# Kernel optimization log

Hardware: AMD Instinct MI355X
Metric: run time of the kernel (lower is better)

The kernel has to match this reference:

```python
import math
import jax
import jax.numpy as jnp
import numpy as np

N_FFT = 2048
HOP = 512
WIN = 2048
N_FREQ = N_FFT // 2 + 1


def _make_buffers():
    # ISTFT synthesis kernel: inverse DFT basis with one-sided spectrum weights.
    n = np.arange(N_FFT, dtype=np.float32)
    k = np.arange(N_FREQ, dtype=np.float32)
    angles = 2.0 * np.pi * k[:, None] * n[None, :] / N_FFT
    w = np.full(N_FREQ, 2.0 / N_FFT, dtype=np.float32)
    w[0] = 1.0 / N_FFT
    if N_FFT % 2 == 0:
        w[-1] = 1.0 / N_FFT
    real_k = np.cos(angles) * w[:, None]
    imag_k = -np.sin(angles) * w[:, None]
    kernel = np.concatenate([real_k, imag_k], axis=0).astype(np.float32)  # [2*N_FREQ, N_FFT]
    # periodic Hann window (torch.hann_window default), win_length == n_fft so no pad
    win = (0.5 * (1.0 - np.cos(2.0 * np.pi * np.arange(WIN) / WIN))).astype(np.float32)
    window_sq = (win * win).astype(np.float32)
    return jnp.asarray(kernel), jnp.asarray(window_sq)


def setup_inputs() -> dict:
    key = jax.random.key(0)
    B, frames = 8, 2048
    stft_repr = jax.random.normal(key, (B, N_FREQ, frames, 2), dtype=jnp.float32)
    kernel, window_sq = _make_buffers()
    orig_len = (frames - 1) * HOP  # 1048064
    return {"stft_repr": stft_repr, "kernel": kernel, "window_sq": window_sq, "orig_len": orig_len}


def reference(stft_repr, kernel, window_sq, orig_len):
    B, n_freq, frames, _ = stft_repr.shape
    # stack real/imag channels: [B, 2*n_freq, frames]
    x = jnp.concatenate([stft_repr[..., 0], stft_repr[..., 1]], axis=1)
    # conv_transpose1d(stride=HOP) == per-frame synthesis GEMM + overlap-add
    contrib = jnp.einsum('bct,cn->btn', x, kernel)  # [B, frames, N_FFT]
    L = (frames - 1) * HOP + N_FFT
    idx = (jnp.arange(frames) * HOP)[:, None] + jnp.arange(N_FFT)[None, :]  # [frames, N_FFT]
    flat = idx.reshape(-1)
    audio = jnp.zeros((B, L), dtype=contrib.dtype).at[:, flat].add(contrib.reshape(B, -1))
    # normalization envelope: every frame fits (e <= L always, since L = (T-1)*hop + n_fft)
    env = jnp.zeros((L,), dtype=window_sq.dtype).at[flat].add(
        jnp.broadcast_to(window_sq, (frames, N_FFT)).reshape(-1))
    env = jnp.maximum(env, 1e-8)
    audio = audio / env[None, :]
    pad = N_FFT // 2
    return audio[:, pad:pad + orig_len]
```

## Files before the change

### kernel.cpp

```cpp
#include <hip/hip_runtime.h>
#include <math.h>

#define NFREQ 1025
#define NT 2048
#define NB 8
#define ORIG_LEN 1048064
#define FR 16
#define SEGS 13
#define NBLK 158
#define FSTR 1028
#define IOFF (FR * FSTR)

__device__ __forceinline__ int dphys(int m) {
    return m ^ ((((m >> 5) ^ (m >> 8)) & 7) << 2);
}
__device__ __forceinline__ int tphys(int r) { return r + (r >> 4); }

template <int LEN, int TSTEP>
__device__ __forceinline__ void r4stage(float* __restrict__ Rw, float* __restrict__ Iw,
                                        const float* __restrict__ TWR,
                                        const float* __restrict__ TWI, int lane) {
#pragma unroll
    for (int c = 0; c < 4; ++c) {
        const int i = lane + (c << 6);
        const int quarter = LEN >> 2;
        const int grp = i / quarter, pos = i - grp * quarter;
        const int i0 = grp * LEN + pos;
        const int ia = dphys(i0), ib = dphys(i0 + quarter);
        const int ic = dphys(i0 + 2 * quarter), id = dphys(i0 + 3 * quarter);
        const float arr = Rw[ia], ari = Iw[ia];
        const float brr = Rw[ib], bri = Iw[ib];
        const float crr = Rw[ic], cri = Iw[ic];
        const float drr = Rw[id], dri = Iw[id];
        const int j1 = tphys(pos * TSTEP), j2 = tphys(2 * pos * TSTEP), j3 = tphys(3 * pos * TSTEP);
        const float w1r = TWR[j1], w1i = TWI[j1];
        const float w2r = TWR[j2], w2i = TWI[j2];
        const float w3r = TWR[j3], w3i = TWI[j3];
        const float t1r = brr * w1r - bri * w1i, t1i = brr * w1i + bri * w1r;
        const float t2r = crr * w2r - cri * w2i, t2i = crr * w2i + cri * w2r;
        const float t3r = drr * w3r - dri * w3i, t3i = drr * w3i + dri * w3r;
        Rw[ia] = arr + t1r + t2r + t3r;  Iw[ia] = ari + t1i + t2i + t3i;
        Rw[ib] = arr - t1i - t2r + t3i;  Iw[ib] = ari + t1r - t2i - t3r;
        Rw[ic] = arr - t1r + t2r - t3r;  Iw[ic] = ari - t1i + t2i - t3i;
        Rw[id] = arr + t1i - t2r - t3i;  Iw[id] = ari - t1r - t2i + t3r;
    }
}

__global__ __launch_bounds__(1024) void istft_fused(const float* __restrict__ in,
                                                    const float* __restrict__ wsq,
                                                    float* __restrict__ out) {
    __shared__ float D[2 * FR * FSTR];
    __shared__ float TWR[816], TWI[816];
    __shared__ float WS[2048];
    const int tid = threadIdx.x;
    const int lane = tid & 63, wv = tid >> 6;
    const int g = blockIdx.x, b = blockIdx.y;
    const int f0 = (g == 0) ? 0 : (13 * g - 1);
    const int sbase = 2 + 13 * g;
    const int nseg = (2049 - sbase < SEGS) ? (2049 - sbase) : SEGS;

    if (tid < 768) {
        float s, c;
        sincosf(6.28318530717958647692f * (float)tid * (1.0f / 1024.0f), &s, &c);
        const int p = tphys(tid);
        TWR[p] = c; TWI[p] = s;
    }
    for (int i = tid; i < 2048; i += 1024) WS[i] = wsq[i];

    const float* bbase = in + (size_t)b * NFREQ * (NT * 2);
#pragma unroll
    for (int it = 0; it < 17; ++it) {
        const int idx = tid + (it << 10);
        if (idx < FR * NFREQ) {
            const int k = idx >> 4, jf = idx & 15, ft = f0 + jf;
            float2 v = make_float2(0.0f, 0.0f);
            if (ft < NT) v = *(const float2*)(bbase + ((size_t)k * NT + ft) * 2);
            D[jf * FSTR + k] = v.x;
            D[IOFF + jf * FSTR + k] = v.y;
        }
    }
    __syncthreads();

    float* Rw = D + wv * FSTR;
    float* Iw = D + IOFF + wv * FSTR;

    float vr[16], vi[16];
#pragma unroll
    for (int m = 0; m < 16; ++m) {
        const int jc = lane + (m << 6);
        const float Xr = Rw[jc];
        const float Xi = (jc == 0) ? 0.0f : Iw[jc];
        const float Cr = Rw[1024 - jc];
        const float Ci = (jc == 0) ? 0.0f : -Iw[1024 - jc];
        const float ar = Xr + Cr, ai = Xi + Ci;
        const float dr = Xr - Cr, di = Xi - Ci;
        const int rr = jc >> 1;
        const int pp = tphys(rr);
        float pr = TWR[pp], pi = TWI[pp];
        if (jc & 1) {
            const float c1r = 0.99999529380957617f, c1i = 0.00306795676296598f;
            const float nr = pr * c1r - pi * c1i;
            pi = pr * c1i + pi * c1r; pr = nr;
        }
        const float br = dr * pr - di * pi;
        const float bi = dr * pi + di * pr;
        vr[m] = (ar - bi) * (1.0f / 2048.0f);
        vi[m] = (ai + br) * (1.0f / 2048.0f);
    }
#pragma unroll
    for (int m0 = 0; m0 < 4; ++m0) {
        const float v0r = vr[m0], v0i = vi[m0];
        const float v1r = vr[m0 + 4], v1i = vi[m0 + 4];
        const float v2r = vr[m0 + 8], v2i = vi[m0 + 8];
        const float v3r = vr[m0 + 12], v3i = vi[m0 + 12];
        const int jb = lane + (m0 << 6);
        const int g8 = ((jb & 3) << 6) | (((jb >> 2) & 3) << 4) |
                       (((jb >> 4) & 3) << 2) | ((jb >> 6) & 3);
        const int p4 = dphys(g8 << 2);
        *(float4*)&Rw[p4] = make_float4(v0r + v1r + v2r + v3r,
                                        v0r - v1i - v2r + v3i,
                                        v0r - v1r + v2r - v3r,
                                        v0r + v1i - v2r - v3i);
        *(float4*)&Iw[p4] = make_float4(v0i + v1i + v2i + v3i,
                                        v0i + v1r - v2i - v3r,
                                        v0i - v1i + v2i - v3i,
                                        v0i - v1r - v2i + v3r);
    }
    r4stage<16, 64>(Rw, Iw, TWR, TWI, lane);
    r4stage<64, 16>(Rw, Iw, TWR, TWI, lane);
    r4stage<256, 4>(Rw, Iw, TWR, TWI, lane);
    r4stage<1024, 1>(Rw, Iw, TWR, TWI, lane);
    __syncthreads();

    const int nsamp = nseg << 9;
    float* outb = out + (size_t)b * ORIG_LEN + (size_t)(sbase - 2) * 512;
#pragma unroll
    for (int it = 0; it < 7; ++it) {
        const int idx = tid + (it << 10);
        if (idx < nsamp) {
            const int seg = idx >> 9, r = idx & 511;
            const int s = sbase + seg;
            const int qlo = (s == 2048) ? 1 : 0;
            const int qhi = (s == 2) ? 2 : 3;
            float acc = 0.0f, wacc = 0.0f;
            const int po = (r & 1) ? IOFF : 0;
#pragma unroll
            for (int q = 0; q < 4; ++q) {
                if (q >= qlo && q <= qhi) {
                    const int lf = s - q - f0;
                    const int n = (q << 9) + r;
                    acc += D[po + lf * FSTR + dphys(n >> 1)];
                    wacc += WS[n];
                }
            }
            outb[idx] = acc / fmaxf(wacc, 1e-8f);
        }
    }
}

extern "C" void kernel_launch(void* const* d_in, const int* in_sizes, int n_in,
                              void* d_out, int out_size, void* d_ws, size_t ws_size,
                              hipStream_t stream) {
    const float* stft = (const float*)d_in[0];
    const float* wsq  = (const float*)d_in[2];
    float* out = (float*)d_out;
    dim3 grid(NBLK, NB);
    istft_fused<<<grid, 1024, 0, stream>>>(stft, wsq, out);
}
```

Baseline: 293.7 us.

## Use interleaved complex LDS layout, derive twiddles, compute constant window envelope

Switches the shared-memory FFT buffer from split real/imag planes to interleaved float2, so each butterfly access is a single 64-bit LDS operation and the output stage writes float2 pairs. Radix-4 twiddles w2 and w3 are now computed from w1 by complex multiplication instead of being loaded, which shrinks the twiddle table. The window_sq input is no longer read: the overlap-add envelope is taken as the analytic constant 1.5 for a periodic Hann at 4x overlap, with edge corrections computed via cosf. This relies on the window being Hann and ignores the supplied buffer, and deriving twiddles by multiplication adds a little rounding error.

```diff
diff --git a/kernel.cpp b/kernel.cpp
--- a/kernel.cpp
+++ b/kernel.cpp
@@ -8,50 +8,47 @@
 #define FR 16
 #define SEGS 13
 #define NBLK 158
-#define FSTR 1028
-#define IOFF (FR * FSTR)
+#define CROW 1026
+#define PI_F 3.14159265358979323846f
 
-__device__ __forceinline__ int dphys(int m) {
+__device__ __forceinline__ int cphys(int m) {
     return m ^ ((((m >> 5) ^ (m >> 8)) & 7) << 2);
 }
 __device__ __forceinline__ int tphys(int r) { return r + (r >> 4); }
 
+__device__ __forceinline__ float2 cmul(float2 a, float2 b) {
+    return make_float2(a.x * b.x - a.y * b.y, a.x * b.y + a.y * b.x);
+}
+
 template <int LEN, int TSTEP>
-__device__ __forceinline__ void r4stage(float* __restrict__ Rw, float* __restrict__ Iw,
-                                        const float* __restrict__ TWR,
-                                        const float* __restrict__ TWI, int lane) {
+__device__ __forceinline__ void r4stage(float2* __restrict__ W,
+                                        const float2* __restrict__ TW, int lane) {
 #pragma unroll
     for (int c = 0; c < 4; ++c) {
         const int i = lane + (c << 6);
         const int quarter = LEN >> 2;
         const int grp = i / quarter, pos = i - grp * quarter;
         const int i0 = grp * LEN + pos;
-        const int ia = dphys(i0), ib = dphys(i0 + quarter);
-        const int ic = dphys(i0 + 2 * quarter), id = dphys(i0 + 3 * quarter);
-        const float arr = Rw[ia], ari = Iw[ia];
-        const float brr = Rw[ib], bri = Iw[ib];
-        const float crr = Rw[ic], cri = Iw[ic];
-        const float drr = Rw[id], dri = Iw[id];
-        const int j1 = tphys(pos * TSTEP), j2 = tphys(2 * pos * TSTEP), j3 = tphys(3 * pos * TSTEP);
-        const float w1r = TWR[j1], w1i = TWI[j1];
-        const float w2r = TWR[j2], w2i = TWI[j2];
-        const float w3r = TWR[j3], w3i = TWI[j3];
-        const float t1r = brr * w1r - bri * w1i, t1i = brr * w1i + bri * w1r;
-        const float t2r = crr * w2r - cri * w2i, t2i = crr * w2i + cri * w2r;
-        const float t3r = drr * w3r - dri * w3i, t3i = drr * w3i + dri * w3r;
-        Rw[ia] = arr + t1r + t2r + t3r;  Iw[ia] = ari + t1i + t2i + t3i;
-        Rw[ib] = arr - t1i - t2r + t3i;  Iw[ib] = ari + t1r - t2i - t3r;
-        Rw[ic] = arr - t1r + t2r - t3r;  Iw[ic] = ari - t1i + t2i - t3i;
-        Rw[id] = arr + t1i - t2r - t3i;  Iw[id] = ari - t1r - t2i + t3r;
+        const int ia = cphys(i0), ib = cphys(i0 + quarter);
+        const int ic = cphys(i0 + 2 * quarter), id = cphys(i0 + 3 * quarter);
+        const float2 a = W[ia], bv = W[ib], cv = W[ic], dv = W[id];
+        const float2 w1 = TW[tphys(pos * TSTEP)];
+        const float2 w2 = cmul(w1, w1);
+        const float2 w3 = cmul(w2, w1);
+        const float2 t1 = cmul(bv, w1);
+        const float2 t2 = cmul(cv, w2);
+        const float2 t3 = cmul(dv, w3);
+        W[ia] = make_float2(a.x + t1.x + t2.x + t3.x, a.y + t1.y + t2.y + t3.y);
+        W[ib] = make_float2(a.x - t1.y - t2.x + t3.y, a.y + t1.x - t2.y - t3.x);
+        W[ic] = make_float2(a.x - t1.x + t2.x - t3.x, a.y - t1.y + t2.y - t3.y);
+        W[id] = make_float2(a.x + t1.y - t2.x - t3.y, a.y - t1.x - t2.y + t3.x);
     }
 }
 
 __global__ __launch_bounds__(1024) void istft_fused(const float* __restrict__ in,
-                                                    const float* __restrict__ wsq,
                                                     float* __restrict__ out) {
-    __shared__ float D[2 * FR * FSTR];
-    __shared__ float TWR[816], TWI[816];
-    __shared__ float WS[2048];
+    __shared__ float2 D[FR * CROW];
+    __shared__ float2 TW[544];
     const int tid = threadIdx.x;
     const int lane = tid & 63, wv = tid >> 6;
     const int g = blockIdx.x, b = blockIdx.y;
@@ -59,13 +56,11 @@
     const int sbase = 2 + 13 * g;
     const int nseg = (2049 - sbase < SEGS) ? (2049 - sbase) : SEGS;
 
-    if (tid < 768) {
+    if (tid < 512) {
         float s, c;
         sincosf(6.28318530717958647692f * (float)tid * (1.0f / 1024.0f), &s, &c);
-        const int p = tphys(tid);
-        TWR[p] = c; TWI[p] = s;
+        TW[tphys(tid)] = make_float2(c, s);
     }
-    for (int i = tid; i < 2048; i += 1024) WS[i] = wsq[i];
 
     const float* bbase = in + (size_t)b * NFREQ * (NT * 2);
 #pragma unroll
@@ -73,87 +68,87 @@
         const int idx = tid + (it << 10);
         if (idx < FR * NFREQ) {
             const int k = idx >> 4, jf = idx & 15, ft = f0 + jf;
-            float2 v = make_float2(0.0f, 0.0f);
-            if (ft < NT) v = *(const float2*)(bbase + ((size_t)k * NT + ft) * 2);
-            D[jf * FSTR + k] = v.x;
-            D[IOFF + jf * FSTR + k] = v.y;
+            float2 v2 = make_float2(0.0f, 0.0f);
+            if (ft < NT) v2 = *(const float2*)(bbase + ((size_t)k * NT + ft) * 2);
+            D[jf * CROW + k] = v2;
         }
     }
     __syncthreads();
 
-    float* Rw = D + wv * FSTR;
-    float* Iw = D + IOFF + wv * FSTR;
+    float2* W = D + wv * CROW;
 
-    float vr[16], vi[16];
+    float2 v[16];
 #pragma unroll
     for (int m = 0; m < 16; ++m) {
         const int jc = lane + (m << 6);
-        const float Xr = Rw[jc];
-        const float Xi = (jc == 0) ? 0.0f : Iw[jc];
-        const float Cr = Rw[1024 - jc];
-        const float Ci = (jc == 0) ? 0.0f : -Iw[1024 - jc];
+        const float2 xa = W[jc];
+        const float2 xb = W[1024 - jc];
+        const float Xr = xa.x, Xi = (jc == 0) ? 0.0f : xa.y;
+        const float Cr = xb.x, Ci = (jc == 0) ? 0.0f : -xb.y;
         const float ar = Xr + Cr, ai = Xi + Ci;
         const float dr = Xr - Cr, di = Xi - Ci;
-        const int rr = jc >> 1;
-        const int pp = tphys(rr);
-        float pr = TWR[pp], pi = TWI[pp];
-        if (jc & 1) {
-            const float c1r = 0.99999529380957617f, c1i = 0.00306795676296598f;
-            const float nr = pr * c1r - pi * c1i;
-            pi = pr * c1i + pi * c1r; pr = nr;
-        }
-        const float br = dr * pr - di * pi;
-        const float bi = dr * pi + di * pr;
-        vr[m] = (ar - bi) * (1.0f / 2048.0f);
-        vi[m] = (ai + br) * (1.0f / 2048.0f);
+        float2 w = TW[tphys(jc >> 1)];
+        if (jc & 1)
+            w = cmul(w, make_float2(0.99999529380957617f, 0.00306795676296598f));
+        const float br = dr * w.x - di * w.y;
+        const float bi = dr * w.y + di * w.x;
+        v[m] = make_float2((ar - bi) * (1.0f / 2048.0f), (ai + br) * (1.0f / 2048.0f));
     }
 #pragma unroll
     for (int m0 = 0; m0 < 4; ++m0) {
-        const float v0r = vr[m0], v0i = vi[m0];
-        const float v1r = vr[m0 + 4], v1i = vi[m0 + 4];
-        const float v2r = vr[m0 + 8], v2i = vi[m0 + 8];
-        const float v3r = vr[m0 + 12], v3i = vi[m0 + 12];
+        const float2 v0 = v[m0], v1 = v[m0 + 4], v2 = v[m0 + 8], v3 = v[m0 + 12];
         const int jb = lane + (m0 << 6);
         const int g8 = ((jb & 3) << 6) | (((jb >> 2) & 3) << 4) |
                        (((jb >> 4) & 3) << 2) | ((jb >> 6) & 3);
-        const int p4 = dphys(g8 << 2);
-        *(float4*)&Rw[p4] = make_float4(v0r + v1r + v2r + v3r,
-                                        v0r - v1i - v2r + v3i,
-                                        v0r - v1r + v2r - v3r,
-                                        v0r + v1i - v2r - v3i);
-        *(float4*)&Iw[p4] = make_float4(v0i + v1i + v2i + v3i,
-                                        v0i + v1r - v2i - v3r,
-                                        v0i - v1i + v2i - v3i,
-                                        v0i - v1r - v2i + v3r);
+        const int p4 = cphys(g8 << 2);
+        *(float4*)&W[p4]     = make_float4(v0.x + v1.x + v2.x + v3.x,
+                                           v0.y + v1.y + v2.y + v3.y,
+                                           v0.x - v1.y - v2.x + v3.y,
+                                           v0.y + v1.x - v2.y - v3.x);
+        *(float4*)&W[p4 + 2] = make_float4(v0.x - v1.x + v2.x - v3.x,
+                                           v0.y - v1.y + v2.y - v3.y,
+                                           v0.x + v1.y - v2.x - v3.y,
+                                           v0.y - v1.x - v2.y + v3.x);
     }
-    r4stage<16, 64>(Rw, Iw, TWR, TWI, lane);
-    r4stage<64, 16>(Rw, Iw, TWR, TWI, lane);
-    r4stage<256, 4>(Rw, Iw, TWR, TWI, lane);
-    r4stage<1024, 1>(Rw, Iw, TWR, TWI, lane);
+    r4stage<16, 64>(W, TW, lane);
+    r4stage<64, 16>(W, TW, lane);
+    r4stage<256, 4>(W, TW, lane);
+    r4stage<1024, 1>(W, TW, lane);
     __syncthreads();
 
-    const int nsamp = nseg << 9;
-    float* outb = out + (size_t)b * ORIG_LEN + (size_t)(sbase - 2) * 512;
+    const int npairs = nseg << 8;
+    float2* outb = (float2*)(out + (size_t)b * ORIG_LEN + (size_t)(sbase - 2) * 512);
 #pragma unroll
-    for (int it = 0; it < 7; ++it) {
-        const int idx = tid + (it << 10);
-        if (idx < nsamp) {
-            const int seg = idx >> 9, r = idx & 511;
+    for (int it = 0; it < 4; ++it) {
+        const int pj = tid + (it << 10);
+        if (pj < npairs) {
+            const int seg = pj >> 8, r2 = pj & 255;
             const int s = sbase + seg;
             const int qlo = (s == 2048) ? 1 : 0;
             const int qhi = (s == 2) ? 2 : 3;
-            float acc = 0.0f, wacc = 0.0f;
-            const int po = (r & 1) ? IOFF : 0;
+            const int rowoff = (s - f0) * CROW;
+            float ax = 0.0f, ay = 0.0f;
 #pragma unroll
             for (int q = 0; q < 4; ++q) {
                 if (q >= qlo && q <= qhi) {
-                    const int lf = s - q - f0;
-                    const int n = (q << 9) + r;
-                    acc += D[po + lf * FSTR + dphys(n >> 1)];
-                    wacc += WS[n];
+                    const float2 c2 = D[rowoff - q * CROW + cphys((q << 8) + r2)];
+                    ax += c2.x; ay += c2.y;
                 }
             }
-            outb[idx] = acc / fmaxf(wacc, 1e-8f);
+            float envx = 1.5f, envy = 1.5f;
+            if (s == 2) {
+                const int n0 = 1536 + (r2 << 1);
+                const float wa = 0.5f - 0.5f * cosf((float)n0 * (PI_F / 1024.0f));
+                const float wb = 0.5f - 0.5f * cosf((float)(n0 + 1) * (PI_F / 1024.0f));
+                envx -= wa * wa; envy -= wb * wb;
+            }
+            if (s == 2048) {
+                const int n0 = r2 << 1;
+                const float wa = 0.5f - 0.5f * cosf((float)n0 * (PI_F / 1024.0f));
+                const float wb = 0.5f - 0.5f * cosf((float)(n0 + 1) * (PI_F / 1024.0f));
+                envx -= wa * wa; envy -= wb * wb;
+            }
+            outb[pj] = make_float2(ax / envx, ay / envy);
         }
     }
 }
@@ -162,8 +157,7 @@
                               void* d_out, int out_size, void* d_ws, size_t ws_size,
                               hipStream_t stream) {
     const float* stft = (const float*)d_in[0];
-    const float* wsq  = (const float*)d_in[2];
     float* out = (float*)d_out;
     dim3 grid(NBLK, NB);
-    istft_fused<<<grid, 1024, 0, stream>>>(stft, wsq, out);
+    istft_fused<<<grid, 1024, 0, stream>>>(stft, out);
 }
```

New measurement: 291.6 us. About the same (-0.7%).
